# Kernel tuning notes

Hardware: AMD Instinct MI355X
Metric: run time of the kernel (lower is better)

The kernel has to match this reference:

```python
import jax, jax.numpy as jnp
import numpy as np


def setup_inputs() -> dict:
    key = jax.random.key(0)
    k1, k2 = jax.random.split(key)
    x = jax.random.normal(k1, (32, 256, 32, 32), dtype=jnp.float32)
    emb = jax.random.uniform(k2, (256, 2048), dtype=jnp.float32)
    return {"x": x, "emb": emb}


def reference(x, emb):
    # x: (B, D, H, W), emb: (D, K)
    B, D = x.shape[0], x.shape[1]
    spatial = x.shape[2:]
    K = emb.shape[1]
    # flatten latents: (N, D) with N = B*H*W
    xf = jnp.moveaxis(x, 1, -1).reshape(-1, D)
    d2 = (jnp.sum(xf * xf, axis=-1, keepdims=True)
          - 2.0 * (xf @ emb)
          + jnp.sum(emb * emb, axis=0))  # (N, K)
    argmin = jnp.argmin(d2, axis=-1)  # (N,)
    q = jnp.take(emb.T, argmin, axis=0)  # (N, D) nearest codes
    out = q.reshape(B, *spatial, D)
    out = jnp.moveaxis(out, -1, 1)  # (B, D, H, W)
    return out
```

## Files before the change

kernel.cpp:

```cpp
#include <hip/hip_runtime.h>


typedef __attribute__((ext_vector_type(8))) _Float16 half8v;
typedef __attribute__((ext_vector_type(16))) float floatx16;
typedef unsigned int uint;
typedef unsigned short ushort;

#define DD 256
#define KK 2048
#define SS 1024
#define NN 32768
#define MT 128
#define NTT 256
#define CD 32
#define LDA 40
#define MFMA_F16 __builtin_amdgcn_mfma_f32_32x32x16_f16

union HU { _Float16 f; ushort u; };
union FragU { uint u[4]; half8v v; };

__device__ __forceinline__ void split16(float v, ushort& h, ushort& l) {
    HU a, b;
    a.f = (_Float16)v;
    b.f = (_Float16)(v - (float)a.f);
    h = a.u; l = b.u;
}

__device__ __forceinline__ uint pk(ushort a, ushort b) {
    return (uint)a | ((uint)b << 16);
}

__global__ __launch_bounds__(256) void hn_kernel(const float* __restrict__ emb,
                                                 float* __restrict__ hn) {
    __shared__ float red[256];
    const int tid = threadIdx.x;
    const int k = blockIdx.x * 32 + (tid & 31);
    const int j = tid >> 5;
    float a = 0.f;
#pragma unroll
    for (int i = 0; i < 32; ++i) {
        float e = emb[(size_t)(j * 32 + i) * KK + k];
        a += e * e;
    }
    red[tid] = a;
    __syncthreads();
    if (j == 0) {
        float s = a;
#pragma unroll
        for (int g = 1; g < 8; ++g) s += red[g * 32 + (tid & 31)];
        hn[k] = 0.5f * s;
    }
}

__global__ __launch_bounds__(256) void pack_emb(const float* __restrict__ emb,
                                                uint4* __restrict__ epk) {
    int idx = blockIdx.x * 256 + threadIdx.x;
    int k = idx & (KK - 1);
    int q = idx >> 11;
    ushort h[8], l[8];
#pragma unroll
    for (int j = 0; j < 8; ++j) {
        float e = emb[(size_t)(8 * q + j) * KK + k];
        split16(e, h[j], l[j]);
    }
    uint4 H, L;
    H.x = pk(h[0], h[1]); H.y = pk(h[2], h[3]);
    H.z = pk(h[4], h[5]); H.w = pk(h[6], h[7]);
    L.x = pk(l[0], l[1]); L.y = pk(l[2], l[3]);
    L.z = pk(l[4], l[5]); L.w = pk(l[6], l[7]);
    epk[(size_t)(q * 2 + 0) * KK + k] = H;
    epk[(size_t)(q * 2 + 1) * KK + k] = L;
}

template <bool PRE>
__global__ __launch_bounds__(1024, 4) void vq_fused(
        const float* __restrict__ x, const float* __restrict__ emb,
        const float* __restrict__ hn, const uint4* __restrict__ epk,
        float* __restrict__ out) {
    __shared__ ushort Bh[2][NTT * LDA], Bl[2][NTT * LDA];
    __shared__ float sv[4][MT];
    __shared__ int   sc[4][MT];
    __shared__ int   bc[MT];

    const int tid = threadIdx.x;
    const int lane = tid & 63;
    const int wid = tid >> 6;
    const int colk = lane & 31;
    const int half = lane >> 5;
    const int wm = (wid & 3) * 32;
    const int wn = (wid >> 2) * 64;

    const int base_n = blockIdx.x * MT;
    const int bq = base_n >> 10;
    const int sb = base_n & (SS - 1);

    const int cod_b = tid & 255;
    const int pB = (tid >> 8) & 1;
    const int oB = tid >> 9;

    const float* xw = x + ((size_t)bq * DD + half * 8) * SS + sb + wm + colk;

    floatx16 acc[2];
#pragma unroll
    for (int j = 0; j < 2; ++j) acc[j] = (floatx16)(0.0f);

    float bestv[16];
    int bestc[16];
#pragma unroll
    for (int r = 0; r < 16; ++r) { bestv[r] = 3.4e38f; bestc[r] = 0; }

    uint4 u00, u01, u10, u11;
    float fb0[16], fb1[16];
    float fa[16];

    auto issueA = [&](int c) {
        const int dt = (c & 7) * CD;
#pragma unroll
        for (int t = 0; t < 2; ++t)
#pragma unroll
            for (int j = 0; j < 8; ++j)
                fa[t * 8 + j] = xw[(size_t)(dt + t * 16 + j) * SS];
    };
    auto issueB = [&](int c, uint4& a0, uint4& a1, float (&fb)[16]) {
        const int kt = c >> 3;
        const int dt = (c & 7) * CD;
        if constexpr (PRE) {
            const int qg = (dt >> 3) + 2 * oB;
            const size_t kb = (size_t)kt * NTT + cod_b;
            a0 = epk[(size_t)(qg * 2 + pB) * KK + kb];
            a1 = epk[(size_t)((qg + 1) * 2 + pB) * KK + kb];
        } else {
#pragma unroll
            for (int i = 0; i < 16; ++i)
                fb[i] = emb[(size_t)(dt + oB * 16 + i) * KK
                            + (size_t)kt * NTT + cod_b];
        }
    };
    auto stageWrite = [&](int nxt, uint4& a0, uint4& a1, float (&fb)[16]) {
        uint4 w0, w1;
        if constexpr (PRE) {
            w0 = a0; w1 = a1;
        } else {
            ushort hh[16], ll[16];
#pragma unroll
            for (int i = 0; i < 16; ++i) split16(fb[i], hh[i], ll[i]);
            const ushort* s = pB ? ll : hh;
            w0.x = pk(s[0], s[1]);   w0.y = pk(s[2], s[3]);
            w0.z = pk(s[4], s[5]);   w0.w = pk(s[6], s[7]);
            w1.x = pk(s[8], s[9]);   w1.y = pk(s[10], s[11]);
            w1.z = pk(s[12], s[13]); w1.w = pk(s[14], s[15]);
        }
        ushort* Bp = pB ? &Bl[nxt][0] : &Bh[nxt][0];
        *reinterpret_cast<uint4*>(&Bp[cod_b * LDA + oB * 16]) = w0;
        *reinterpret_cast<uint4*>(&Bp[cod_b * LDA + oB * 16 + 8]) = w1;
    };
    auto compute = [&](int cur) {
        const int fo = colk * LDA + half * 8;
#pragma unroll
        for (int t = 0; t < 2; ++t) {
            ushort h[8], l[8];
#pragma unroll
            for (int j = 0; j < 8; ++j) split16(fa[t * 8 + j], h[j], l[j]);
            FragU ah, al;
#pragma unroll
            for (int j = 0; j < 4; ++j) {
                ah.u[j] = pk(h[2 * j], h[2 * j + 1]);
                al.u[j] = pk(l[2 * j], l[2 * j + 1]);
            }
            const int o = t * 16;
            half8v bh0 = *reinterpret_cast<const half8v*>(&Bh[cur][fo + wn * LDA + o]);
            half8v bh1 = *reinterpret_cast<const half8v*>(&Bh[cur][fo + (wn + 32) * LDA + o]);
            half8v bl0 = *reinterpret_cast<const half8v*>(&Bl[cur][fo + wn * LDA + o]);
            half8v bl1 = *reinterpret_cast<const half8v*>(&Bl[cur][fo + (wn + 32) * LDA + o]);

            acc[0] = MFMA_F16(ah.v, bh0, acc[0], 0, 0, 0);
            acc[0] = MFMA_F16(ah.v, bl0, acc[0], 0, 0, 0);
            acc[0] = MFMA_F16(al.v, bh0, acc[0], 0, 0, 0);

            acc[1] = MFMA_F16(ah.v, bh1, acc[1], 0, 0, 0);
            acc[1] = MFMA_F16(ah.v, bl1, acc[1], 0, 0, 0);
            acc[1] = MFMA_F16(al.v, bh1, acc[1], 0, 0, 0);
        }
    };
    auto epilogue = [&](int kt) {
        const int cd0 = kt * NTT + wn + colk;
        const int cd1 = cd0 + 32;
        const float h0 = hn[cd0];
        const float h1 = hn[cd1];
#pragma unroll
        for (int r = 0; r < 16; ++r) {
            float s0 = h0 - acc[0][r];
            float s1 = h1 - acc[1][r];
            float v = s0; int cd = cd0;
            if (s1 < s0) { v = s1; cd = cd1; }
            if (v < bestv[r]) { bestv[r] = v; bestc[r] = cd; }
            acc[0][r] = 0.f;
            acc[1][r] = 0.f;
        }
    };

    issueB(0, u00, u01, fb0);
    stageWrite(0, u00, u01, fb0);
    issueB(1, u10, u11, fb1);
    __syncthreads();

    for (int cc = 0; cc < 32; ++cc) {
        const int c0 = cc * 2;
        if (c0 + 2 < 64) { issueB(c0 + 2, u00, u01, fb0); }
        issueA(c0);
        stageWrite(1, u10, u11, fb1);
        compute(0);
        __syncthreads();

        const int c1 = c0 + 1;
        if (c1 + 2 < 64) { issueB(c1 + 2, u10, u11, fb1); }
        issueA(c1);
        if (c1 + 1 < 64) { stageWrite(0, u00, u01, fb0); }
        compute(1);
        if ((c1 & 7) == 7) epilogue(c1 >> 3);
        __syncthreads();
    }

#pragma unroll
    for (int r = 0; r < 16; ++r) {
        float v = bestv[r];
        int cd = bestc[r];
#pragma unroll
        for (int mk = 1; mk < 32; mk <<= 1) {
            float ov = __shfl_xor(v, mk);
            int oc = __shfl_xor(cd, mk);
            if (ov < v || (ov == v && oc < cd)) { v = ov; cd = oc; }
        }
        if (colk == 0) {
            const int row = (r & 3) + 8 * (r >> 2) + 4 * half;
            sv[wid >> 2][wm + row] = v;
            sc[wid >> 2][wm + row] = cd;
        }
    }
    __syncthreads();
    if (tid < MT) {
        float v = sv[0][tid]; int cd = sc[0][tid];
#pragma unroll
        for (int g = 1; g < 4; ++g) {
            float ov = sv[g][tid]; int oc = sc[g][tid];
            if (ov < v || (ov == v && oc < cd)) { v = ov; cd = oc; }
        }
        bc[tid] = cd;
    }
    __syncthreads();
    {
        const int mq = tid & 31;
        const int dg = tid >> 5;
        const int k0 = bc[mq * 4 + 0];
        const int k1 = bc[mq * 4 + 1];
        const int k2 = bc[mq * 4 + 2];
        const int k3 = bc[mq * 4 + 3];
#pragma unroll 4
        for (int dd = 0; dd < 8; ++dd) {
            const int d = dg * 8 + dd;
            const float* er = emb + (size_t)d * KK;
            float4 o = make_float4(er[k0], er[k1], er[k2], er[k3]);
            reinterpret_cast<float4*>(&out[((size_t)bq * DD + d) * SS + sb])[mq] = o;
        }
    }
}

extern "C" void kernel_launch(void* const* d_in, const int* in_sizes, int n_in,
                              void* d_out, int out_size, void* d_ws, size_t ws_size,
                              hipStream_t stream) {
    const float* x = (const float*)d_in[0];
    const float* emb = (const float*)d_in[1];
    float* out = (float*)d_out;
    float* hn = (float*)d_ws;
    uint4* epk = (uint4*)((char*)d_ws + KK * sizeof(float));

    const size_t need = (size_t)KK * 4 + (size_t)32 * 2 * KK * 16;

    hipLaunchKernelGGL(hn_kernel, dim3(KK / 32), dim3(256), 0, stream, emb, hn);
    if (ws_size >= need) {
        hipLaunchKernelGGL(pack_emb, dim3(65536 / 256), dim3(256), 0, stream,
                           emb, epk);
        hipLaunchKernelGGL((vq_fused<true>), dim3(NN / MT), dim3(1024), 0, stream,
                           x, emb, hn, epk, out);
    } else {
        hipLaunchKernelGGL((vq_fused<false>), dim3(NN / MT), dim3(1024), 0, stream,
                           x, emb, hn, epk, out);
    }
}
```

Measured before the change: 223.8 us.

## Stage split A tiles in LDS and use 2x2 warp tiles with 512 threads

```diff
diff --git a/kernel.cpp b/kernel.cpp
--- a/kernel.cpp
+++ b/kernel.cpp
@@ -17,7 +17,6 @@
 #define MFMA_F16 __builtin_amdgcn_mfma_f32_32x32x16_f16
 
 union HU { _Float16 f; ushort u; };
-union FragU { uint u[4]; half8v v; };
 
 __device__ __forceinline__ void split16(float v, ushort& h, ushort& l) {
     HU a, b;
@@ -28,6 +27,11 @@
 
 __device__ __forceinline__ uint pk(ushort a, ushort b) {
     return (uint)a | ((uint)b << 16);
+}
+
+__device__ __forceinline__ void barrier_nodrain() {
+    asm volatile("s_waitcnt lgkmcnt(0)" ::: "memory");
+    __builtin_amdgcn_s_barrier();
 }
 
 __global__ __launch_bounds__(256) void hn_kernel(const float* __restrict__ emb,
@@ -73,10 +77,11 @@
 }
 
 template <bool PRE>
-__global__ __launch_bounds__(1024, 4) void vq_fused(
+__global__ __launch_bounds__(512, 2) void vq_fused(
         const float* __restrict__ x, const float* __restrict__ emb,
         const float* __restrict__ hn, const uint4* __restrict__ epk,
         float* __restrict__ out) {
+    __shared__ ushort Ah[2][MT * LDA], Al[2][MT * LDA];
     __shared__ ushort Bh[2][NTT * LDA], Bl[2][NTT * LDA];
     __shared__ float sv[4][MT];
     __shared__ int   sc[4][MT];
@@ -87,99 +92,119 @@
     const int wid = tid >> 6;
     const int colk = lane & 31;
     const int half = lane >> 5;
-    const int wm = (wid & 3) * 32;
-    const int wn = (wid >> 2) * 64;
+    const int wm = (wid & 1) * 64;
+    const int wn = (wid >> 1) * 64;
 
     const int base_n = blockIdx.x * MT;
     const int bq = base_n >> 10;
     const int sb = base_n & (SS - 1);
 
+    const int lat_a = (tid & 15) + 16 * (tid >> 6);
+    const int qa2 = (tid >> 4) & 3;
     const int cod_b = tid & 255;
-    const int pB = (tid >> 8) & 1;
-    const int oB = tid >> 9;
-
-    const float* xw = x + ((size_t)bq * DD + half * 8) * SS + sb + wm + colk;
-
-    floatx16 acc[2];
-#pragma unroll
-    for (int j = 0; j < 2; ++j) acc[j] = (floatx16)(0.0f);
-
-    float bestv[16];
-    int bestc[16];
-#pragma unroll
-    for (int r = 0; r < 16; ++r) { bestv[r] = 3.4e38f; bestc[r] = 0; }
-
-    uint4 u00, u01, u10, u11;
-    float fb0[16], fb1[16];
-    float fa[16];
-
-    auto issueA = [&](int c) {
+    const int pB = tid >> 8;
+
+    const float* xA = x + ((size_t)bq * DD + 8 * qa2) * SS + sb + lat_a;
+
+    floatx16 acc[2][2];
+#pragma unroll
+    for (int i = 0; i < 2; ++i)
+#pragma unroll
+        for (int j = 0; j < 2; ++j) acc[i][j] = (floatx16)(0.0f);
+
+    float bestv[2][16];
+    int bestc[2][16];
+#pragma unroll
+    for (int t = 0; t < 2; ++t)
+#pragma unroll
+        for (int r = 0; r < 16; ++r) { bestv[t][r] = 3.4e38f; bestc[t][r] = 0; }
+
+    float fa0[8], fa1[8];
+    uint4 ub0[4], ub1[4];
+    float fb0[32], fb1[32];
+
+    auto issueA = [&](int c, float (&fa)[8]) {
         const int dt = (c & 7) * CD;
 #pragma unroll
-        for (int t = 0; t < 2; ++t)
-#pragma unroll
-            for (int j = 0; j < 8; ++j)
-                fa[t * 8 + j] = xw[(size_t)(dt + t * 16 + j) * SS];
-    };
-    auto issueB = [&](int c, uint4& a0, uint4& a1, float (&fb)[16]) {
+        for (int j = 0; j < 8; ++j) fa[j] = xA[(size_t)(dt + j) * SS];
+    };
+    auto issueB = [&](int c, uint4 (&ub)[4], float (&fb)[32]) {
         const int kt = c >> 3;
         const int dt = (c & 7) * CD;
         if constexpr (PRE) {
-            const int qg = (dt >> 3) + 2 * oB;
+            const int qg = dt >> 3;
             const size_t kb = (size_t)kt * NTT + cod_b;
-            a0 = epk[(size_t)(qg * 2 + pB) * KK + kb];
-            a1 = epk[(size_t)((qg + 1) * 2 + pB) * KK + kb];
+#pragma unroll
+            for (int s = 0; s < 4; ++s)
+                ub[s] = epk[(size_t)((qg + s) * 2 + pB) * KK + kb];
         } else {
 #pragma unroll
-            for (int i = 0; i < 16; ++i)
-                fb[i] = emb[(size_t)(dt + oB * 16 + i) * KK
-                            + (size_t)kt * NTT + cod_b];
-        }
-    };
-    auto stageWrite = [&](int nxt, uint4& a0, uint4& a1, float (&fb)[16]) {
-        uint4 w0, w1;
+            for (int i = 0; i < 32; ++i)
+                fb[i] = emb[(size_t)(dt + i) * KK + (size_t)kt * NTT + cod_b];
+        }
+    };
+    auto stageWrite = [&](int nxt, float (&fa)[8], uint4 (&ub)[4],
+                          float (&fb)[32]) {
+        ushort h[8], l[8];
+#pragma unroll
+        for (int j = 0; j < 8; ++j) split16(fa[j], h[j], l[j]);
+        uint4 H, L;
+        H.x = pk(h[0], h[1]); H.y = pk(h[2], h[3]);
+        H.z = pk(h[4], h[5]); H.w = pk(h[6], h[7]);
+        L.x = pk(l[0], l[1]); L.y = pk(l[2], l[3]);
+        L.z = pk(l[4], l[5]); L.w = pk(l[6], l[7]);
+        *reinterpret_cast<uint4*>(&Ah[nxt][lat_a * LDA + 8 * qa2]) = H;
+        *reinterpret_cast<uint4*>(&Al[nxt][lat_a * LDA + 8 * qa2]) = L;
+        ushort* Bp = pB ? &Bl[nxt][0] : &Bh[nxt][0];
         if constexpr (PRE) {
-            w0 = a0; w1 = a1;
+#pragma unroll
+            for (int s = 0; s < 4; ++s)
+                *reinterpret_cast<uint4*>(&Bp[cod_b * LDA + 8 * s]) = ub[s];
         } else {
-            ushort hh[16], ll[16];
-#pragma unroll
-            for (int i = 0; i < 16; ++i) split16(fb[i], hh[i], ll[i]);
-            const ushort* s = pB ? ll : hh;
-            w0.x = pk(s[0], s[1]);   w0.y = pk(s[2], s[3]);
-            w0.z = pk(s[4], s[5]);   w0.w = pk(s[6], s[7]);
-            w1.x = pk(s[8], s[9]);   w1.y = pk(s[10], s[11]);
-            w1.z = pk(s[12], s[13]); w1.w = pk(s[14], s[15]);
-        }
-        ushort* Bp = pB ? &Bl[nxt][0] : &Bh[nxt][0];
-        *reinterpret_cast<uint4*>(&Bp[cod_b * LDA + oB * 16]) = w0;
-        *reinterpret_cast<uint4*>(&Bp[cod_b * LDA + oB * 16 + 8]) = w1;
+            ushort hh[32], ll[32];
+#pragma unroll
+            for (int i = 0; i < 32; ++i) split16(fb[i], hh[i], ll[i]);
+            const ushort* s_ = pB ? ll : hh;
+#pragma unroll
+            for (int s = 0; s < 4; ++s) {
+                uint4 w;
+                w.x = pk(s_[8 * s + 0], s_[8 * s + 1]);
+                w.y = pk(s_[8 * s + 2], s_[8 * s + 3]);
+                w.z = pk(s_[8 * s + 4], s_[8 * s + 5]);
+                w.w = pk(s_[8 * s + 6], s_[8 * s + 7]);
+                *reinterpret_cast<uint4*>(&Bp[cod_b * LDA + 8 * s]) = w;
+            }
+        }
     };
     auto compute = [&](int cur) {
         const int fo = colk * LDA + half * 8;
 #pragma unroll
         for (int t = 0; t < 2; ++t) {
-            ushort h[8], l[8];
-#pragma unroll
-            for (int j = 0; j < 8; ++j) split16(fa[t * 8 + j], h[j], l[j]);
-            FragU ah, al;
-#pragma unroll
-            for (int j = 0; j < 4; ++j) {
-                ah.u[j] = pk(h[2 * j], h[2 * j + 1]);
-                al.u[j] = pk(l[2 * j], l[2 * j + 1]);
-            }
             const int o = t * 16;
+            half8v ah0 = *reinterpret_cast<const half8v*>(&Ah[cur][fo + wm * LDA + o]);
+            half8v ah1 = *reinterpret_cast<const half8v*>(&Ah[cur][fo + (wm + 32) * LDA + o]);
+            half8v al0 = *reinterpret_cast<const half8v*>(&Al[cur][fo + wm * LDA + o]);
+            half8v al1 = *reinterpret_cast<const half8v*>(&Al[cur][fo + (wm + 32) * LDA + o]);
             half8v bh0 = *reinterpret_cast<const half8v*>(&Bh[cur][fo + wn * LDA + o]);
             half8v bh1 = *reinterpret_cast<const half8v*>(&Bh[cur][fo + (wn + 32) * LDA + o]);
             half8v bl0 = *reinterpret_cast<const half8v*>(&Bl[cur][fo + wn * LDA + o]);
             half8v bl1 = *reinterpret_cast<const half8v*>(&Bl[cur][fo + (wn + 32) * LDA + o]);
 
-            acc[0] = MFMA_F16(ah.v, bh0, acc[0], 0, 0, 0);
-            acc[0] = MFMA_F16(ah.v, bl0, acc[0], 0, 0, 0);
-            acc[0] = MFMA_F16(al.v, bh0, acc[0], 0, 0, 0);
-
-            acc[1] = MFMA_F16(ah.v, bh1, acc[1], 0, 0, 0);
-            acc[1] = MFMA_F16(ah.v, bl1, acc[1], 0, 0, 0);
-            acc[1] = MFMA_F16(al.v, bh1, acc[1], 0, 0, 0);
+            acc[0][0] = MFMA_F16(ah0, bh0, acc[0][0], 0, 0, 0);
+            acc[0][0] = MFMA_F16(ah0, bl0, acc[0][0], 0, 0, 0);
+            acc[0][0] = MFMA_F16(al0, bh0, acc[0][0], 0, 0, 0);
+
+            acc[0][1] = MFMA_F16(ah0, bh1, acc[0][1], 0, 0, 0);
+            acc[0][1] = MFMA_F16(ah0, bl1, acc[0][1], 0, 0, 0);
+            acc[0][1] = MFMA_F16(al0, bh1, acc[0][1], 0, 0, 0);
+
+            acc[1][0] = MFMA_F16(ah1, bh0, acc[1][0], 0, 0, 0);
+            acc[1][0] = MFMA_F16(ah1, bl0, acc[1][0], 0, 0, 0);
+            acc[1][0] = MFMA_F16(al1, bh0, acc[1][0], 0, 0, 0);
+
+            acc[1][1] = MFMA_F16(ah1, bh1, acc[1][1], 0, 0, 0);
+            acc[1][1] = MFMA_F16(ah1, bl1, acc[1][1], 0, 0, 0);
+            acc[1][1] = MFMA_F16(al1, bh1, acc[1][1], 0, 0, 0);
         }
     };
     auto epilogue = [&](int kt) {
@@ -188,53 +213,57 @@
         const float h0 = hn[cd0];
         const float h1 = hn[cd1];
 #pragma unroll
-        for (int r = 0; r < 16; ++r) {
-            float s0 = h0 - acc[0][r];
-            float s1 = h1 - acc[1][r];
-            float v = s0; int cd = cd0;
-            if (s1 < s0) { v = s1; cd = cd1; }
-            if (v < bestv[r]) { bestv[r] = v; bestc[r] = cd; }
-            acc[0][r] = 0.f;
-            acc[1][r] = 0.f;
-        }
-    };
-
-    issueB(0, u00, u01, fb0);
-    stageWrite(0, u00, u01, fb0);
-    issueB(1, u10, u11, fb1);
-    __syncthreads();
+        for (int tm = 0; tm < 2; ++tm) {
+#pragma unroll
+            for (int r = 0; r < 16; ++r) {
+                float s0 = h0 - acc[tm][0][r];
+                float s1 = h1 - acc[tm][1][r];
+                float v = s0; int cd = cd0;
+                if (s1 < s0) { v = s1; cd = cd1; }
+                if (v < bestv[tm][r]) { bestv[tm][r] = v; bestc[tm][r] = cd; }
+                acc[tm][0][r] = 0.f;
+                acc[tm][1][r] = 0.f;
+            }
+        }
+    };
+
+    issueA(0, fa0); issueB(0, ub0, fb0);
+    stageWrite(0, fa0, ub0, fb0);
+    issueA(1, fa1); issueB(1, ub1, fb1);
+    barrier_nodrain();
 
     for (int cc = 0; cc < 32; ++cc) {
         const int c0 = cc * 2;
-        if (c0 + 2 < 64) { issueB(c0 + 2, u00, u01, fb0); }
-        issueA(c0);
-        stageWrite(1, u10, u11, fb1);
+        if (c0 + 2 < 64) { issueA(c0 + 2, fa0); issueB(c0 + 2, ub0, fb0); }
+        stageWrite(1, fa1, ub1, fb1);
         compute(0);
-        __syncthreads();
+        barrier_nodrain();
 
         const int c1 = c0 + 1;
-        if (c1 + 2 < 64) { issueB(c1 + 2, u10, u11, fb1); }
-        issueA(c1);
-        if (c1 + 1 < 64) { stageWrite(0, u00, u01, fb0); }
+        if (c1 + 2 < 64) { issueA(c1 + 2, fa1); issueB(c1 + 2, ub1, fb1); }
+        if (c1 + 1 < 64) { stageWrite(0, fa0, ub0, fb0); }
         compute(1);
         if ((c1 & 7) == 7) epilogue(c1 >> 3);
-        __syncthreads();
-    }
-
-#pragma unroll
-    for (int r = 0; r < 16; ++r) {
-        float v = bestv[r];
-        int cd = bestc[r];
-#pragma unroll
-        for (int mk = 1; mk < 32; mk <<= 1) {
-            float ov = __shfl_xor(v, mk);
-            int oc = __shfl_xor(cd, mk);
-            if (ov < v || (ov == v && oc < cd)) { v = ov; cd = oc; }
-        }
-        if (colk == 0) {
-            const int row = (r & 3) + 8 * (r >> 2) + 4 * half;
-            sv[wid >> 2][wm + row] = v;
-            sc[wid >> 2][wm + row] = cd;
+        barrier_nodrain();
+    }
+
+#pragma unroll
+    for (int tm = 0; tm < 2; ++tm) {
+#pragma unroll
+        for (int r = 0; r < 16; ++r) {
+            float v = bestv[tm][r];
+            int cd = bestc[tm][r];
+#pragma unroll
+            for (int mk = 1; mk < 32; mk <<= 1) {
+                float ov = __shfl_xor(v, mk);
+                int oc = __shfl_xor(cd, mk);
+                if (ov < v || (ov == v && oc < cd)) { v = ov; cd = oc; }
+            }
+            if (colk == 0) {
+                const int row = (r & 3) + 8 * (r >> 2) + 4 * half;
+                sv[wid >> 1][wm + tm * 32 + row] = v;
+                sc[wid >> 1][wm + tm * 32 + row] = cd;
+            }
         }
     }
     __syncthreads();
@@ -256,8 +285,8 @@
         const int k2 = bc[mq * 4 + 2];
         const int k3 = bc[mq * 4 + 3];
 #pragma unroll 4
-        for (int dd = 0; dd < 8; ++dd) {
-            const int d = dg * 8 + dd;
+        for (int dd = 0; dd < 16; ++dd) {
+            const int d = dg * 16 + dd;
             const float* er = emb + (size_t)d * KK;
             float4 o = make_float4(er[k0], er[k1], er[k2], er[k3]);
             reinterpret_cast<float4*>(&out[((size_t)bq * DD + d) * SS + sb])[mq] = o;
@@ -280,10 +309,10 @@
     if (ws_size >= need) {
         hipLaunchKernelGGL(pack_emb, dim3(65536 / 256), dim3(256), 0, stream,
                            emb, epk);
-        hipLaunchKernelGGL((vq_fused<true>), dim3(NN / MT), dim3(1024), 0, stream,
+        hipLaunchKernelGGL((vq_fused<true>), dim3(NN / MT), dim3(512), 0, stream,
                            x, emb, hn, epk, out);
     } else {
-        hipLaunchKernelGGL((vq_fused<false>), dim3(NN / MT), dim3(1024), 0, stream,
+        hipLaunchKernelGGL((vq_fused<false>), dim3(NN / MT), dim3(512), 0, stream,
                            x, emb, hn, epk, out);
     }
 }
```

Measured after the change: 272.1 us. 21.6% more time.
